# Kernel tuning notes

Hardware: AMD Instinct MI355X
Metric: run time of the kernel (lower is better)

## Reference

```python
import jax, jax.numpy as jnp
import numpy as np
from jax import lax

B, T, D, H = 4, 2048, 1024, 8
DK = D // H        # head qk dim (expand_k=1.0) = 128
DV = 2 * D // H    # head v dim (expand_v=2.0) = 256
C = 64             # retention chunk size


def setup_inputs() -> dict:
    key = jax.random.key(0)
    ks = jax.random.split(key, 7)
    s = 0.02
    return {
        "x": jax.random.normal(ks[0], (B, T, D), jnp.float32),
        "Wq": jax.random.normal(ks[1], (D, H * DK), jnp.float32) * s,
        "Wk": jax.random.normal(ks[2], (D, H * DK), jnp.float32) * s,
        "Wv": jax.random.normal(ks[3], (D, H * DV), jnp.float32) * s,
        "Wg": jax.random.normal(ks[4], (D, H * DV), jnp.float32) * s,
        "Wo": jax.random.normal(ks[5], (H * DV, D), jnp.float32) * s,
        "norm_w": jnp.ones((DV,), jnp.float32),
    }


def _rope(x):
    # x: [B,T,H,DK]; GPT-NeoX style (non-interleaved) rotary, base 10000
    half = DK // 2
    inv = 1.0 / (10000.0 ** (jnp.arange(0, DK, 2, dtype=jnp.float32) / DK))
    f = jnp.arange(T, dtype=jnp.float32)[:, None] * inv[None, :]  # [T, half]
    cos = jnp.cos(f)[None, :, None, :]
    sin = jnp.sin(f)[None, :, None, :]
    x1, x2 = x[..., :half], x[..., half:]
    return jnp.concatenate([x1 * cos - x2 * sin, x2 * cos + x1 * sin], axis=-1)


def _retention(q, k, v):
    # chunked decay-gated linear attention (RetNet retention)
    # q,k: [B,T,H,DK], v: [B,T,H,DV]; recurrence S_t = g*S_{t-1} + k_t^T v_t, o_t = q_t S_t
    N = T // C
    gamma = 1.0 - 2.0 ** (-5.0 - jnp.arange(H, dtype=jnp.float32))  # [H] per-head decay
    i = jnp.arange(C, dtype=jnp.float32)
    expo = i[:, None] - i[None, :]                                   # [C,C]
    M = jnp.where(expo >= 0, gamma[:, None, None] ** expo[None], 0.0)  # [H,C,C] intra-chunk decay mask
    dec_q = gamma[:, None] ** (i + 1.0)        # [H,C] decay of state seen by q_i
    dec_k = gamma[:, None] ** (C - 1.0 - i)    # [H,C] decay of k_j into end-of-chunk state
    gC = gamma ** C

    def to_chunks(t):
        return t.reshape(B, N, C, H, -1).transpose(1, 0, 3, 2, 4)  # [N,B,H,C,d]

    qs, kcs, vcs = to_chunks(q), to_chunks(k), to_chunks(v)

    def step(S, inp):
        qc, kc, vc = inp  # [B,H,C,DK],[B,H,C,DK],[B,H,C,DV]
        attn = jnp.einsum('bhid,bhjd->bhij', qc, kc) * M[None]
        o_intra = jnp.einsum('bhij,bhje->bhie', attn, vc)
        o_inter = jnp.einsum('bhid,bhde->bhie', qc, S) * dec_q[None, :, :, None]
        kv = jnp.einsum('bhjd,bhje->bhde', kc * dec_k[None, :, :, None], vc)
        S_new = gC[None, :, None, None] * S + kv
        return S_new, o_intra + o_inter

    S0 = jnp.zeros((B, H, DK, DV), q.dtype)
    _, os_ = lax.scan(step, S0, (qs, kcs, vcs))  # os_: [N,B,H,C,DV]
    return os_.transpose(1, 0, 3, 2, 4).reshape(B, T, H, DV)


def reference(x, Wq, Wk, Wv, Wg, Wo, norm_w):
    q = (x @ Wq).reshape(B, T, H, DK)
    k = (x @ Wk).reshape(B, T, H, DK)
    v = (x @ Wv).reshape(B, T, H, DV)
    g = (x @ Wg).reshape(B, T, H, DV)
    q, k = _rope(q), _rope(k)
    q = q * (DK ** -0.5)
    o = _retention(q, k, v)
    # fused per-head RMSNorm + swish output gate (FusedRMSNormSwishGate)
    rms = jnp.sqrt(jnp.mean(o * o, axis=-1, keepdims=True) + 1e-5)
    o = (o / rms) * norm_w
    o = o * g * jax.nn.sigmoid(g)
    return o.reshape(B, T, H * DV) @ Wo
```

## Files before the change

### kernel.cpp

```cpp
#include <hip/hip_runtime.h>
#include <hip/hip_bf16.h>
#include <cstdint>
#include <cstddef>

using f32x4 = __attribute__((ext_vector_type(4))) float;
using s16x8 = __attribute__((ext_vector_type(8))) short;
using s16x4 = __attribute__((ext_vector_type(4))) short;

#define DEVINL __device__ __forceinline__

static constexpr int T_LEN  = 2048;
static constexpr int MROWS  = 8192;
static constexpr int NCHUNK = 32;

DEVINL float bf2f(short s){
  unsigned u = ((unsigned)(unsigned short)s) << 16;
  return __builtin_bit_cast(float, u);
}
DEVINL short f2bf(float f){
  unsigned u = __builtin_bit_cast(unsigned, f);
  u = (u + 0x7fffu + ((u >> 16) & 1u)) >> 16;
  return (short)(unsigned short)u;
}

#define GLOAD16(gp, lp) \
  __builtin_amdgcn_global_load_lds((__attribute__((address_space(1))) void*)(gp), \
                                   (__attribute__((address_space(3))) void*)(lp), 16, 0, 0)

#define MFMA16(a, b, c) __builtin_amdgcn_mfma_f32_16x16x32_bf16((a), (b), (c), 0, 0, 0)
#define SBAR()  __builtin_amdgcn_sched_barrier(0)
#define WAITLGKM(n) asm volatile("s_waitcnt lgkmcnt(" #n ")" ::: "memory")
#define WAITVM(n)   asm volatile("s_waitcnt vmcnt(" #n ")" ::: "memory")

__global__ __launch_bounds__(256) void cvt_f32_bf16(const float* __restrict__ in,
                                                    short* __restrict__ out, int n4){
  int i = blockIdx.x * 256 + threadIdx.x;
  if (i >= n4) return;
  float4 v = ((const float4*)in)[i];
  short4 o;
  o.x = f2bf(v.x); o.y = f2bf(v.y); o.z = f2bf(v.z); o.w = f2bf(v.w);
  ((short4*)out)[i] = o;
}

__global__ __launch_bounds__(256) void tr_w(const float* __restrict__ in,
                                            short* __restrict__ out, int R, int C){
  __shared__ float tile[32][33];
  int c0 = blockIdx.x * 32, r0 = blockIdx.y * 32;
  int tx = threadIdx.x, ty = threadIdx.y;
  #pragma unroll
  for (int i = 0; i < 4; ++i){
    int r = ty + i * 8;
    tile[r][tx] = in[(size_t)(r0 + r) * C + c0 + tx];
  }
  __syncthreads();
  #pragma unroll
  for (int i = 0; i < 4; ++i){
    int c = ty + i * 8;
    out[(size_t)(c0 + c) * R + r0 + tx] = f2bf(tile[tx][c]);
  }
}

__global__ __launch_bounds__(256) void tr_k_decay(const short* __restrict__ in,
                                                  short* __restrict__ out){
  __shared__ float tile[32][33];
  int c0 = blockIdx.x * 32, r0 = blockIdx.y * 32;
  int tx = threadIdx.x, ty = threadIdx.y;
  #pragma unroll
  for (int i = 0; i < 4; ++i){
    int r = ty + i * 8;
    tile[r][tx] = bf2f(in[(size_t)(r0 + r) * 1024 + c0 + tx]);
  }
  __syncthreads();
  #pragma unroll
  for (int i = 0; i < 4; ++i){
    int c  = c0 + ty + i * 8;
    int h  = c >> 7;
    float lg = log2f(1.0f - exp2f(-(float)(5 + h)));
    int srow = r0 + tx;
    int j = srow & 63;
    float dec = exp2f((float)(63 - j) * lg);
    out[(size_t)c * MROWS + srow] = f2bf(tile[tx][ty + i * 8] * dec);
  }
}

__global__ __launch_bounds__(256) void rope_table(float* __restrict__ tab){
  int i = blockIdx.x * 256 + threadIdx.x;
  int t = i >> 6, d = i & 63;
  float inv = exp2f(-(float)d * (13.287712379549449f / 64.0f));
  float f = (float)t * inv;
  float s, c;
  sincosf(f, &s, &c);
  tab[2 * i]     = c;
  tab[2 * i + 1] = s;
}

__global__ __launch_bounds__(256) void rope_inplace(short* __restrict__ qk,
                                                    const float* __restrict__ tab,
                                                    float scale, int bake){
  int idx = blockIdx.x * 256 + threadIdx.x;
  int bt  = idx >> 9, rem = idx & 511;
  int h   = rem >> 6, d = rem & 63;
  int t   = bt & (T_LEN - 1);
  float2 cs = ((const float2*)tab)[t * 64 + d];
  float mult = scale;
  if (bake){
    float lg = log2f(1.0f - exp2f(-(float)(5 + h)));
    mult *= exp2f((float)((t & 63) + 1) * lg);
  }
  size_t base = (size_t)bt * 1024 + h * 128 + d;
  float x1 = bf2f(qk[base]), x2 = bf2f(qk[base + 64]);
  qk[base]      = f2bf((x1 * cs.x - x2 * cs.y) * mult);
  qk[base + 64] = f2bf((x2 * cs.x + x1 * cs.y) * mult);
}

DEVINL s16x8 frag64(const short* buf, int row, int ks, int lhi){
  int ch = (ks * 4 + lhi) ^ (row & 7);
  return *(const s16x8*)&buf[row * 64 + ch * 8];
}

template<int MODE>
__global__ __launch_bounds__(512, 2) void gemm256(const short* __restrict__ A,
                                                  const short* __restrict__ Bt,
                                                  void* __restrict__ o0, void* __restrict__ o1,
                                                  void* __restrict__ o2, void* __restrict__ o3,
                                                  int K, int nt, int NT){
  constexpr int BM   = (MODE == 2 ? 128 : 256);
  constexpr int ABUF = BM * 64;
  constexpr int MF   = BM / 32;
  constexpr int RPP  = MF / 4;
  __shared__ alignas(16) short LBUF[3 * ABUF + 2 * 16384];
  short* const BB = LBUF + 3 * ABUF;
  const int tid = threadIdx.x, wave = tid >> 6, lane = tid & 63;
  const int l15 = lane & 15, lhi = lane >> 4;
  const int wm = (wave >> 2) * (BM / 2), wn = (wave & 3) * 64;
  const int MG  = (gridDim.x >> 3) / NT;
  const int xcd = blockIdx.x & 7, idx = blockIdx.x >> 3;
  const int mi  = idx % MG, nn = idx / MG;
  const int m0  = (xcd * MG + mi) * BM, n0 = nn * 256;
  const short* Ag = A + (size_t)m0 * K;
  const short* Bg = Bt + (size_t)n0 * K;
  const int sr = lane >> 3;
  const int gc = ((lane & 7) ^ sr) * 8;
  const bool vreg = (MODE == 3) && (n0 >= 2048 && n0 < 4096);
  f32x4 acc[MF][4] = {};

  auto stageA = [&](int t, int half){
    short* lb = LBUF + (t % 3) * ABUF;
    size_t k0 = (size_t)t * 64;
    if constexpr (BM == 256){
      #pragma unroll
      for (int c = 0; c < 2; ++c){
        int r0 = half * 128 + c * 64;
        GLOAD16(Ag + (size_t)(r0 + wave * 8 + sr) * K + k0 + gc, lb + (r0 + wave * 8) * 64);
      }
    } else {
      int r0 = half * 64;
      GLOAD16(Ag + (size_t)(r0 + wave * 8 + sr) * K + k0 + gc, lb + (r0 + wave * 8) * 64);
    }
  };
  auto stageB = [&](int t, int half){
    short* lb = BB + (t & 1) * 16384;
    size_t k0 = (size_t)t * 64;
    #pragma unroll
    for (int c = 0; c < 2; ++c){
      int r0 = half * 128 + c * 64;
      GLOAD16(Bg + (size_t)(r0 + wave * 8 + sr) * K + k0 + gc, lb + (r0 + wave * 8) * 64);
    }
  };

  s16x8 bfr[2][4];
  s16x8 afA[RPP][2], afB[RPP][2];
  auto readAf = [&](s16x8 (&dst)[RPP][2], const short* Ab, int q){
    #pragma unroll
    for (int i = 0; i < RPP; ++i)
      #pragma unroll
      for (int ks = 0; ks < 2; ++ks)
        dst[i][ks] = frag64(Ab, wm + (RPP * q + i) * 16 + l15, ks, lhi);
  };
  auto readB = [&](const short* Bb){
    #pragma unroll
    for (int ks = 0; ks < 2; ++ks)
      #pragma unroll
      for (int nf = 0; nf < 4; ++nf)
        bfr[ks][nf] = frag64(Bb, wn + nf * 16 + l15, ks, lhi);
  };

  stageA(0, 0); stageA(0, 1); stageB(0, 0); stageB(0, 1);
  stageA(1, 0); stageA(1, 1); stageB(1, 0); stageB(1, 1);
  if constexpr (BM == 256) WAITVM(8); else WAITVM(6);
  SBAR();
  __builtin_amdgcn_s_barrier();
  readAf(afA, LBUF, 0);

  for (int t = 0; t < nt; ++t){
    const short* Ab  = LBUF + (t % 3) * ABUF;
    const short* Anx = LBUF + ((t + 1) % 3) * ABUF;
    const short* Bb  = BB + (t & 1) * 16384;
    #pragma unroll
    for (int q = 0; q < 4; ++q){
      __builtin_amdgcn_s_barrier();
      if (q == 2){
        if (t + 2 < nt){ if constexpr (BM == 256) WAITVM(4); else WAITVM(2); }
        else           { WAITVM(0); }
        SBAR();
      }
      if (t + 2 < nt){
        if (q == 0) stageA(t + 2, 0);
        if (q == 1) stageA(t + 2, 1);
        if (q == 2) stageB(t + 2, 0);
        if (q == 3) stageB(t + 2, 1);
      }
      bool tail = (q == 3) && (t + 1 >= nt);
      if (q == 0){ readB(Bb); SBAR(); readAf(afB, Ab, 1); }
      else if (q == 1){ readAf(afA, Ab, 2); }
      else if (q == 2){ readAf(afB, Ab, 3); }
      else if (!tail) { readAf(afA, Anx, 0); }
      if (tail){ WAITLGKM(0); }
      else if constexpr (RPP == 2){ WAITLGKM(4); }
      else                        { WAITLGKM(2); }
      SBAR();
      __builtin_amdgcn_s_setprio(1);
      if (vreg){
        #pragma unroll
        for (int i = 0; i < RPP; ++i)
          #pragma unroll
          for (int nf = 0; nf < 4; ++nf)
            #pragma unroll
            for (int ks = 0; ks < 2; ++ks)
              acc[RPP * q + i][nf] = (q & 1)
                ? MFMA16(afB[i][ks], bfr[ks][nf], acc[RPP * q + i][nf])
                : MFMA16(afA[i][ks], bfr[ks][nf], acc[RPP * q + i][nf]);
      } else {
        #pragma unroll
        for (int i = 0; i < RPP; ++i)
          #pragma unroll
          for (int nf = 0; nf < 4; ++nf)
            #pragma unroll
            for (int ks = 0; ks < 2; ++ks)
              acc[RPP * q + i][nf] = (q & 1)
                ? MFMA16(bfr[ks][nf], afB[i][ks], acc[RPP * q + i][nf])
                : MFMA16(bfr[ks][nf], afA[i][ks], acc[RPP * q + i][nf]);
      }
      __builtin_amdgcn_s_setprio(0);
    }
  }
  if (MODE == 2){
    float* dst = (float*)o0;
    #pragma unroll
    for (int mf = 0; mf < MF; ++mf){
      int m = m0 + wm + mf * 16 + l15;
      #pragma unroll
      for (int nf = 0; nf < 4; ++nf){
        int nb = n0 + wn + nf * 16 + 4 * lhi;
        *(float4*)&dst[(size_t)m * 1024 + nb] = *(float4*)&acc[mf][nf];
      }
    }
  } else if (vreg){
    short* dst = (short*)o2;
    #pragma unroll
    for (int mf = 0; mf < MF; ++mf){
      int rb = m0 + wm + mf * 16 + 4 * lhi;
      #pragma unroll
      for (int nf = 0; nf < 4; ++nf){
        int e = (n0 - 2048) + wn + nf * 16 + l15;
        s16x4 pk;
        #pragma unroll
        for (int r = 0; r < 4; ++r) pk[r] = f2bf(acc[mf][nf][r]);
        *(s16x4*)&dst[(size_t)e * MROWS + rb] = pk;
      }
    }
  } else {
    short* dst; int ld, cb;
    if (n0 < 1024)      { dst = (short*)o0; ld = 1024; cb = n0; }
    else if (n0 < 2048) { dst = (short*)o1; ld = 1024; cb = n0 - 1024; }
    else                { dst = (short*)o3; ld = 2048; cb = n0 - 4096; }
    #pragma unroll
    for (int mf = 0; mf < MF; ++mf){
      int m = m0 + wm + mf * 16 + l15;
      #pragma unroll
      for (int nf = 0; nf < 4; ++nf){
        int nb = cb + wn + nf * 16 + 4 * lhi;
        s16x4 pk;
        #pragma unroll
        for (int r = 0; r < 4; ++r) pk[r] = f2bf(acc[mf][nf][r]);
        *(s16x4*)&dst[(size_t)m * ld + nb] = pk;
      }
    }
  }
}

__global__ __launch_bounds__(256) void ret_scan(const short* __restrict__ kT,
                                                const short* __restrict__ vT,
                                                short* __restrict__ ST){
  __shared__ alignas(16) short kbuf[3][4096];
  __shared__ alignas(16) short vbuf[3][4096];
  const int tid = threadIdx.x, wave = tid >> 6, lane = tid & 63;
  const int db = blockIdx.x & 1, eb = blockIdx.x >> 1;
  const int h = blockIdx.y, b = blockIdx.z;
  const int d0 = db * 64, e0 = eb * 64;
  const float lg = log2f(1.0f - exp2f(-(float)(5 + h)));
  const float gC = exp2f(64.0f * lg);
  f32x4 Sacc[4] = {};
  const int srow = wave * 8 + (lane >> 3);
  const int sc   = lane & 7;

  auto STAGE = [&](int n, int buf){
    size_t rowbase = (size_t)(b * T_LEN + n * 64);
    #pragma unroll
    for (int c = 0; c < 2; ++c){
      int r = c * 32 + srow;
      int gc2 = sc ^ (r & 7);
      GLOAD16(kT + (size_t)(h * 128 + d0 + r) * MROWS + rowbase + gc2 * 8,
              &kbuf[buf][c * 2048 + wave * 512]);
    }
    #pragma unroll
    for (int c = 0; c < 2; ++c){
      int r = c * 32 + srow;
      int gc2 = sc ^ (r & 7);
      GLOAD16(vT + (size_t)(h * 256 + e0 + r) * MROWS + rowbase + gc2 * 8,
              &vbuf[buf][c * 2048 + wave * 512]);
    }
  };

  STAGE(0, 0);
  STAGE(1, 1);
  for (int n = 0; n < NCHUNK; ++n){
    const int buf = n % 3;
    if (n + 2 < NCHUNK) STAGE(n + 2, (n + 2) % 3);
    if (n > 0){
      size_t stb = (((size_t)n * 4 + b) * 8 + h) * 32768;
      int dbase = d0 + 16 * wave + 4 * (lane >> 4);
      #pragma unroll
      for (int nf = 0; nf < 4; ++nf){
        int e = e0 + nf * 16 + (lane & 15);
        s16x4 pk;
        #pragma unroll
        for (int r = 0; r < 4; ++r) pk[r] = f2bf(Sacc[nf][r]);
        *(s16x4*)&ST[stb + (size_t)e * 128 + dbase] = pk;
      }
    }
    if (n == 0)       WAITVM(8);
    else if (n < 30)  WAITVM(12);
    else if (n == 30) WAITVM(8);
    else              WAITVM(4);
    __builtin_amdgcn_s_barrier();
    SBAR();
    #pragma unroll
    for (int nf = 0; nf < 4; ++nf)
      #pragma unroll
      for (int r = 0; r < 4; ++r) Sacc[nf][r] *= gC;
    #pragma unroll
    for (int ks = 0; ks < 2; ++ks){
      int d = 16 * wave + (lane & 15);
      int chA = (ks * 4 + (lane >> 4)) ^ (d & 7);
      s16x8 af = *(const s16x8*)&kbuf[buf][d * 64 + chA * 8];
      #pragma unroll
      for (int nf = 0; nf < 4; ++nf){
        int e = nf * 16 + (lane & 15);
        int chB = (ks * 4 + (lane >> 4)) ^ (e & 7);
        s16x8 bv = *(const s16x8*)&vbuf[buf][e * 64 + chB * 8];
        Sacc[nf] = MFMA16(af, bv, Sacc[nf]);
      }
    }
    __builtin_amdgcn_s_barrier();
    SBAR();
  }
}

__global__ __launch_bounds__(256, 2) void ret_fused(const short* __restrict__ q,
                                                    const short* __restrict__ k,
                                                    const short* __restrict__ vT,
                                                    const short* __restrict__ ST,
                                                    const short* __restrict__ g,
                                                    const float* __restrict__ nw,
                                                    short* __restrict__ y){
  __shared__ alignas(16) short GS[16384];
  __shared__ alignas(16) float SS[256];
  __shared__ alignas(16) short XS[16896];
  short* PS = XS;
  short* YT = XS;
  const int tid = threadIdx.x, wave = tid >> 6, lane = tid & 63;
  const int l15 = lane & 15, lhi = lane >> 4;
  const int n = blockIdx.x, h = blockIdx.y, b = blockIdx.z;
  const size_t rowbase = (size_t)(b * T_LEN + n * 64);
  {
    int row = wave * 2 + (lane >> 5), sc32 = lane & 31;
    #pragma unroll
    for (int c = 0; c < 8; ++c){
      int r = c * 8 + row;
      GLOAD16(g + (rowbase + r) * 2048 + h * 256 + sc32 * 8, &GS[c * 2048 + wave * 512]);
    }
  }
  s16x8 Qf[4][4];
  #pragma unroll
  for (int rf = 0; rf < 4; ++rf)
    #pragma unroll
    for (int ks = 0; ks < 4; ++ks)
      Qf[rf][ks] = *(const s16x8*)&q[(rowbase + rf * 16 + l15) * 1024 + h * 128 + ks * 32 + lhi * 8];
  s16x8 Kf[4];
  #pragma unroll
  for (int ks = 0; ks < 4; ++ks)
    Kf[ks] = *(const s16x8*)&k[(rowbase + wave * 16 + l15) * 1024 + h * 128 + ks * 32 + lhi * 8];
  f32x4 accP[4] = {};
  #pragma unroll
  for (int ks = 0; ks < 4; ++ks)
    #pragma unroll
    for (int nf = 0; nf < 4; ++nf)
      accP[nf] = MFMA16(Kf[ks], Qf[nf][ks], accP[nf]);
  const float lg = log2f(1.0f - exp2f(-(float)(5 + h)));
  {
    int jb = wave * 16 + 4 * lhi;
    float dj[4];
    #pragma unroll
    for (int r = 0; r < 4; ++r) dj[r] = exp2f(-(float)(jb + r + 1) * lg);
    #pragma unroll
    for (int nf = 0; nf < 4; ++nf){
      int i = nf * 16 + l15;
      s16x4 pk;
      #pragma unroll
      for (int r = 0; r < 4; ++r)
        pk[r] = f2bf((i >= jb + r) ? accP[nf][r] * dj[r] : 0.0f);
      *(s16x4*)&PS[i * 72 + jb] = pk;
    }
  }
  f32x4 acc[4][4] = {};
  if (n){
    size_t stb = (((size_t)n * 4 + b) * 8 + h) * 32768;
    #pragma unroll
    for (int ks = 0; ks < 4; ++ks){
      s16x8 Sf[4];
      #pragma unroll
      for (int nf = 0; nf < 4; ++nf){
        int e = wave * 64 + nf * 16 + l15;
        Sf[nf] = *(const s16x8*)&ST[stb + (size_t)e * 128 + ks * 32 + lhi * 8];
      }
      #pragma unroll
      for (int mf = 0; mf < 4; ++mf)
        #pragma unroll
        for (int nf = 0; nf < 4; ++nf)
          acc[mf][nf] = MFMA16(Qf[mf][ks], Sf[nf], acc[mf][nf]);
    }
  }
  s16x8 Vf[2][4];
  #pragma unroll
  for (int ks2 = 0; ks2 < 2; ++ks2)
    #pragma unroll
    for (int nf = 0; nf < 4; ++nf){
      int e = wave * 64 + nf * 16 + l15;
      Vf[ks2][nf] = *(const s16x8*)&vT[(size_t)(h * 256 + e) * MROWS + rowbase + ks2 * 32 + lhi * 8];
    }
  __syncthreads();
  #pragma unroll
  for (int ks2 = 0; ks2 < 2; ++ks2){
    s16x8 Pf[4];
    #pragma unroll
    for (int mf = 0; mf < 4; ++mf)
      Pf[mf] = *(const s16x8*)&PS[(mf * 16 + l15) * 72 + ks2 * 32 + lhi * 8];
    #pragma unroll
    for (int mf = 0; mf < 4; ++mf)
      #pragma unroll
      for (int nf = 0; nf < 4; ++nf)
        acc[mf][nf] = MFMA16(Pf[mf], Vf[ks2][nf], acc[mf][nf]);
  }
  float ssp[4][4];
  #pragma unroll
  for (int mf = 0; mf < 4; ++mf)
    #pragma unroll
    for (int r = 0; r < 4; ++r){
      float s = 0.f;
      #pragma unroll
      for (int nf = 0; nf < 4; ++nf) s += acc[mf][nf][r] * acc[mf][nf][r];
      #pragma unroll
      for (int off = 8; off >= 1; off >>= 1) s += __shfl_xor(s, off, 64);
      ssp[mf][r] = s;
    }
  if (l15 == 0){
    #pragma unroll
    for (int mf = 0; mf < 4; ++mf)
      #pragma unroll
      for (int r = 0; r < 4; ++r){
        int row = mf * 16 + 4 * lhi + r;
        SS[row * 4 + wave] = ssp[mf][r];
      }
  }
  __syncthreads();
  #pragma unroll
  for (int mf = 0; mf < 4; ++mf){
    float rr[4];
    #pragma unroll
    for (int r = 0; r < 4; ++r){
      int row = mf * 16 + 4 * lhi + r;
      f32x4 s4 = *(const f32x4*)&SS[row * 4];
      float tot = s4[0] + s4[1] + s4[2] + s4[3];
      rr[r] = __builtin_amdgcn_rsqf(tot * (1.0f / 256.0f) + 1e-5f);
    }
    #pragma unroll
    for (int nf = 0; nf < 4; ++nf){
      int e = wave * 64 + nf * 16 + l15;
      float nwe = nw[e];
      #pragma unroll
      for (int r = 0; r < 4; ++r){
        int row = mf * 16 + 4 * lhi + r;
        float gf = bf2f(GS[row * 256 + e]);
        float sig = __builtin_amdgcn_rcpf(1.0f + exp2f(gf * -1.4426950408889634f));
        YT[row * 264 + e] = f2bf(acc[mf][nf][r] * rr[r] * nwe * gf * sig);
      }
    }
  }
  __syncthreads();
  #pragma unroll
  for (int it = 0; it < 8; ++it){
    int flat = it * 2048 + tid * 8;
    int row = flat >> 8, e = flat & 255;
    s16x8 v = *(const s16x8*)&YT[row * 264 + e];
    *(s16x8*)&y[(rowbase + row) * 2048 + h * 256 + e] = v;
  }
}

extern "C" void kernel_launch(void* const* d_in, const int* in_sizes, int n_in,
                              void* d_out, int out_size, void* d_ws, size_t ws_size,
                              hipStream_t stream){
  const float* x  = (const float*)d_in[0];
  const float* Wq = (const float*)d_in[1];
  const float* Wk = (const float*)d_in[2];
  const float* Wv = (const float*)d_in[3];
  const float* Wg = (const float*)d_in[4];
  const float* Wo = (const float*)d_in[5];
  const float* nw = (const float*)d_in[6];
  float* out = (float*)d_out;

  char* w = (char*)d_ws;
  short* xb  = (short*)w;               w += (size_t)8192 * 1024 * 2;
  short* WT  = (short*)w;               w += (size_t)6144 * 1024 * 2;
  short* kTt = (short*)w;               w += (size_t)1024 * 8192 * 2;
  short* qb  = (short*)w;               w += (size_t)8192 * 1024 * 2;
  short* kb  = (short*)w;               w += (size_t)8192 * 1024 * 2;
  short* vT  = (short*)w;               w += (size_t)2048 * 8192 * 2;
  short* gb  = (short*)w;               w += (size_t)8192 * 2048 * 2;
  short* STb = (short*)w;               w += (size_t)32 * 4 * 8 * 32768 * 2;
  short* WoT = (short*)w;               w += (size_t)1024 * 2048 * 2;
  short* yb  = (short*)d_ws;
  float* tab = (float*)STb;

  cvt_f32_bf16<<<8192, 256, 0, stream>>>(x, xb, 8192 * 1024 / 4);
  dim3 tb(32, 8);
  tr_w<<<dim3(32, 32), tb, 0, stream>>>(Wq, WT,                       1024, 1024);
  tr_w<<<dim3(32, 32), tb, 0, stream>>>(Wk, WT + (size_t)1024 * 1024, 1024, 1024);
  tr_w<<<dim3(64, 32), tb, 0, stream>>>(Wv, WT + (size_t)2048 * 1024, 1024, 2048);
  tr_w<<<dim3(64, 32), tb, 0, stream>>>(Wg, WT + (size_t)4096 * 1024, 1024, 2048);
  tr_w<<<dim3(32, 64), tb, 0, stream>>>(Wo, WoT,                      2048, 1024);
  rope_table<<<512, 256, 0, stream>>>(tab);

  gemm256<3><<<768, 512, 0, stream>>>(xb, WT, qb, kb, vT, gb, 1024, 16, 24);

  rope_inplace<<<16384, 256, 0, stream>>>(qb, tab, 0.08838834764831845f, 1);
  rope_inplace<<<16384, 256, 0, stream>>>(kb, tab, 1.0f, 0);
  tr_k_decay<<<dim3(32, 256), tb, 0, stream>>>(kb, kTt);

  ret_scan <<<dim3(8, 8, 4),  256, 0, stream>>>(kTt, vT, STb);
  ret_fused<<<dim3(32, 8, 4), 256, 0, stream>>>(qb, kb, vT, STb, gb, nw, yb);

  gemm256<2><<<256, 512, 0, stream>>>(yb, WoT, out, nullptr, nullptr, nullptr, 2048, 32, 4);
}
```

Before: 311.4 us.

## Split projection GEMM, merge weight transposes and rope launches, simplify GEMM pipeline

Merges the four QKVG weight transposes into one launch and the two RoPE launches into one 2D-grid launch. Reorders WT so Wg sits before Wv, and splits the fused QKVG GEMM into a q/k/g GEMM plus a separate MODE-4 GEMM that writes transposed v. This removes the runtime vreg branch. The GEMM main loop drops the register double-buffered A-fragment prefetch and uses simpler per-quarter fragment loads with a full LDS wait and barriers. That may lose overlap of LDS reads with MFMA work.

```diff
diff --git a/kernel.cpp b/kernel.cpp
--- a/kernel.cpp
+++ b/kernel.cpp
@@ -57,6 +57,33 @@
   for (int i = 0; i < 4; ++i){
     int c = ty + i * 8;
     out[(size_t)(c0 + c) * R + r0 + tx] = f2bf(tile[tx][c]);
+  }
+}
+
+__global__ __launch_bounds__(256) void tr_w4(const float* __restrict__ Wq,
+                                             const float* __restrict__ Wk,
+                                             const float* __restrict__ Wv,
+                                             const float* __restrict__ Wg,
+                                             short* __restrict__ WT){
+  __shared__ float tile[32][33];
+  int bx = blockIdx.x;
+  const float* src; int C; size_t off; int cb;
+  if (bx < 32)       { src = Wq; C = 1024; off = 0;                       cb = bx; }
+  else if (bx < 64)  { src = Wk; C = 1024; off = (size_t)1024 * 1024;     cb = bx - 32; }
+  else if (bx < 128) { src = Wg; C = 2048; off = (size_t)2048 * 1024;     cb = bx - 64; }
+  else               { src = Wv; C = 2048; off = (size_t)4096 * 1024;     cb = bx - 128; }
+  int c0 = cb * 32, r0 = blockIdx.y * 32;
+  int tx = threadIdx.x, ty = threadIdx.y;
+  #pragma unroll
+  for (int i = 0; i < 4; ++i){
+    int r = ty + i * 8;
+    tile[r][tx] = src[(size_t)(r0 + r) * C + c0 + tx];
+  }
+  __syncthreads();
+  #pragma unroll
+  for (int i = 0; i < 4; ++i){
+    int c = ty + i * 8;
+    WT[off + (size_t)(c0 + c) * 1024 + r0 + tx] = f2bf(tile[tx][c]);
   }
 }
 
@@ -94,23 +121,25 @@
   tab[2 * i + 1] = s;
 }
 
-__global__ __launch_bounds__(256) void rope_inplace(short* __restrict__ qk,
-                                                    const float* __restrict__ tab,
-                                                    float scale, int bake){
+__global__ __launch_bounds__(256) void rope2(short* __restrict__ qb, short* __restrict__ kb,
+                                             const float* __restrict__ tab){
   int idx = blockIdx.x * 256 + threadIdx.x;
   int bt  = idx >> 9, rem = idx & 511;
   int h   = rem >> 6, d = rem & 63;
   int t   = bt & (T_LEN - 1);
   float2 cs = ((const float2*)tab)[t * 64 + d];
-  float mult = scale;
-  if (bake){
+  short* dst; float mult;
+  if (blockIdx.y == 0){
+    dst = qb;
     float lg = log2f(1.0f - exp2f(-(float)(5 + h)));
-    mult *= exp2f((float)((t & 63) + 1) * lg);
+    mult = 0.08838834764831845f * exp2f((float)((t & 63) + 1) * lg);
+  } else {
+    dst = kb; mult = 1.0f;
   }
   size_t base = (size_t)bt * 1024 + h * 128 + d;
-  float x1 = bf2f(qk[base]), x2 = bf2f(qk[base + 64]);
-  qk[base]      = f2bf((x1 * cs.x - x2 * cs.y) * mult);
-  qk[base + 64] = f2bf((x2 * cs.x + x1 * cs.y) * mult);
+  float x1 = bf2f(dst[base]), x2 = bf2f(dst[base + 64]);
+  dst[base]      = f2bf((x1 * cs.x - x2 * cs.y) * mult);
+  dst[base + 64] = f2bf((x2 * cs.x + x1 * cs.y) * mult);
 }
 
 DEVINL s16x8 frag64(const short* buf, int row, int ks, int lhi){
@@ -141,7 +170,6 @@
   const short* Bg = Bt + (size_t)n0 * K;
   const int sr = lane >> 3;
   const int gc = ((lane & 7) ^ sr) * 8;
-  const bool vreg = (MODE == 3) && (n0 >= 2048 && n0 < 4096);
   f32x4 acc[MF][4] = {};
 
   auto stageA = [&](int t, int half){
@@ -166,23 +194,6 @@
       int r0 = half * 128 + c * 64;
       GLOAD16(Bg + (size_t)(r0 + wave * 8 + sr) * K + k0 + gc, lb + (r0 + wave * 8) * 64);
     }
-  };
-
-  s16x8 bfr[2][4];
-  s16x8 afA[RPP][2], afB[RPP][2];
-  auto readAf = [&](s16x8 (&dst)[RPP][2], const short* Ab, int q){
-    #pragma unroll
-    for (int i = 0; i < RPP; ++i)
-      #pragma unroll
-      for (int ks = 0; ks < 2; ++ks)
-        dst[i][ks] = frag64(Ab, wm + (RPP * q + i) * 16 + l15, ks, lhi);
-  };
-  auto readB = [&](const short* Bb){
-    #pragma unroll
-    for (int ks = 0; ks < 2; ++ks)
-      #pragma unroll
-      for (int nf = 0; nf < 4; ++nf)
-        bfr[ks][nf] = frag64(Bb, wn + nf * 16 + l15, ks, lhi);
   };
 
   stageA(0, 0); stageA(0, 1); stageB(0, 0); stageB(0, 1);
@@ -190,61 +201,61 @@
   if constexpr (BM == 256) WAITVM(8); else WAITVM(6);
   SBAR();
   __builtin_amdgcn_s_barrier();
-  readAf(afA, LBUF, 0);
 
   for (int t = 0; t < nt; ++t){
-    const short* Ab  = LBUF + (t % 3) * ABUF;
-    const short* Anx = LBUF + ((t + 1) % 3) * ABUF;
-    const short* Bb  = BB + (t & 1) * 16384;
+    const short* Ab = LBUF + (t % 3) * ABUF;
+    const short* Bb = BB + (t & 1) * 16384;
+    s16x8 bfr[2][4];
     #pragma unroll
     for (int q = 0; q < 4; ++q){
-      __builtin_amdgcn_s_barrier();
-      if (q == 2){
-        if (t + 2 < nt){ if constexpr (BM == 256) WAITVM(4); else WAITVM(2); }
-        else           { WAITVM(0); }
-        SBAR();
-      }
+      if (q == 0){
+        #pragma unroll
+        for (int ks = 0; ks < 2; ++ks)
+          #pragma unroll
+          for (int nf = 0; nf < 4; ++nf)
+            bfr[ks][nf] = frag64(Bb, wn + nf * 16 + l15, ks, lhi);
+      }
+      s16x8 af[RPP][2];
+      #pragma unroll
+      for (int i = 0; i < RPP; ++i)
+        #pragma unroll
+        for (int ks = 0; ks < 2; ++ks)
+          af[i][ks] = frag64(Ab, wm + (RPP * q + i) * 16 + l15, ks, lhi);
       if (t + 2 < nt){
         if (q == 0) stageA(t + 2, 0);
         if (q == 1) stageA(t + 2, 1);
         if (q == 2) stageB(t + 2, 0);
         if (q == 3) stageB(t + 2, 1);
       }
-      bool tail = (q == 3) && (t + 1 >= nt);
-      if (q == 0){ readB(Bb); SBAR(); readAf(afB, Ab, 1); }
-      else if (q == 1){ readAf(afA, Ab, 2); }
-      else if (q == 2){ readAf(afB, Ab, 3); }
-      else if (!tail) { readAf(afA, Anx, 0); }
-      if (tail){ WAITLGKM(0); }
-      else if constexpr (RPP == 2){ WAITLGKM(4); }
-      else                        { WAITLGKM(2); }
+      SBAR();
+      __builtin_amdgcn_s_barrier();
+      WAITLGKM(0);
       SBAR();
       __builtin_amdgcn_s_setprio(1);
-      if (vreg){
-        #pragma unroll
-        for (int i = 0; i < RPP; ++i)
+      #pragma unroll
+      for (int i = 0; i < RPP; ++i)
+        #pragma unroll
+        for (int nf = 0; nf < 4; ++nf)
           #pragma unroll
-          for (int nf = 0; nf < 4; ++nf)
-            #pragma unroll
-            for (int ks = 0; ks < 2; ++ks)
-              acc[RPP * q + i][nf] = (q & 1)
-                ? MFMA16(afB[i][ks], bfr[ks][nf], acc[RPP * q + i][nf])
-                : MFMA16(afA[i][ks], bfr[ks][nf], acc[RPP * q + i][nf]);
-      } else {
-        #pragma unroll
-        for (int i = 0; i < RPP; ++i)
-          #pragma unroll
-          for (int nf = 0; nf < 4; ++nf)
-            #pragma unroll
-            for (int ks = 0; ks < 2; ++ks)
-              acc[RPP * q + i][nf] = (q & 1)
-                ? MFMA16(bfr[ks][nf], afB[i][ks], acc[RPP * q + i][nf])
-                : MFMA16(bfr[ks][nf], afA[i][ks], acc[RPP * q + i][nf]);
-      }
+          for (int ks = 0; ks < 2; ++ks){
+            if constexpr (MODE == 4)
+              acc[RPP * q + i][nf] = MFMA16(af[i][ks], bfr[ks][nf], acc[RPP * q + i][nf]);
+            else
+              acc[RPP * q + i][nf] = MFMA16(bfr[ks][nf], af[i][ks], acc[RPP * q + i][nf]);
+          }
       __builtin_amdgcn_s_setprio(0);
-    }
-  }
-  if (MODE == 2){
+      if (q == 3){
+        if (t < nt - 2){
+          if constexpr (BM == 256) WAITVM(8); else WAITVM(6);
+        } else if (t == nt - 2){
+          WAITVM(0);
+        }
+        SBAR();
+      }
+      __builtin_amdgcn_s_barrier();
+    }
+  }
+  if constexpr (MODE == 2){
     float* dst = (float*)o0;
     #pragma unroll
     for (int mf = 0; mf < MF; ++mf){
@@ -255,14 +266,14 @@
         *(float4*)&dst[(size_t)m * 1024 + nb] = *(float4*)&acc[mf][nf];
       }
     }
-  } else if (vreg){
+  } else if constexpr (MODE == 4){
     short* dst = (short*)o2;
     #pragma unroll
     for (int mf = 0; mf < MF; ++mf){
       int rb = m0 + wm + mf * 16 + 4 * lhi;
       #pragma unroll
       for (int nf = 0; nf < 4; ++nf){
-        int e = (n0 - 2048) + wn + nf * 16 + l15;
+        int e = n0 + wn + nf * 16 + l15;
         s16x4 pk;
         #pragma unroll
         for (int r = 0; r < 4; ++r) pk[r] = f2bf(acc[mf][nf][r]);
@@ -273,7 +284,7 @@
     short* dst; int ld, cb;
     if (n0 < 1024)      { dst = (short*)o0; ld = 1024; cb = n0; }
     else if (n0 < 2048) { dst = (short*)o1; ld = 1024; cb = n0 - 1024; }
-    else                { dst = (short*)o3; ld = 2048; cb = n0 - 4096; }
+    else                { dst = (short*)o3; ld = 2048; cb = n0 - 2048; }
     #pragma unroll
     for (int mf = 0; mf < MF; ++mf){
       int m = m0 + wm + mf * 16 + l15;
@@ -544,17 +555,15 @@
 
   cvt_f32_bf16<<<8192, 256, 0, stream>>>(x, xb, 8192 * 1024 / 4);
   dim3 tb(32, 8);
-  tr_w<<<dim3(32, 32), tb, 0, stream>>>(Wq, WT,                       1024, 1024);
-  tr_w<<<dim3(32, 32), tb, 0, stream>>>(Wk, WT + (size_t)1024 * 1024, 1024, 1024);
-  tr_w<<<dim3(64, 32), tb, 0, stream>>>(Wv, WT + (size_t)2048 * 1024, 1024, 2048);
-  tr_w<<<dim3(64, 32), tb, 0, stream>>>(Wg, WT + (size_t)4096 * 1024, 1024, 2048);
-  tr_w<<<dim3(32, 64), tb, 0, stream>>>(Wo, WoT,                      2048, 1024);
+  tr_w4<<<dim3(192, 32), tb, 0, stream>>>(Wq, Wk, Wv, Wg, WT);
+  tr_w <<<dim3(32, 64),  tb, 0, stream>>>(Wo, WoT, 2048, 1024);
   rope_table<<<512, 256, 0, stream>>>(tab);
 
-  gemm256<3><<<768, 512, 0, stream>>>(xb, WT, qb, kb, vT, gb, 1024, 16, 24);
-
-  rope_inplace<<<16384, 256, 0, stream>>>(qb, tab, 0.08838834764831845f, 1);
-  rope_inplace<<<16384, 256, 0, stream>>>(kb, tab, 1.0f, 0);
+  gemm256<3><<<512, 512, 0, stream>>>(xb, WT, qb, kb, nullptr, gb, 1024, 16, 16);
+  gemm256<4><<<256, 512, 0, stream>>>(xb, WT + (size_t)4096 * 1024, nullptr, nullptr, vT, nullptr,
+                                      1024, 16, 8);
+
+  rope2<<<dim3(16384, 2), 256, 0, stream>>>(qb, kb, tab);
   tr_k_decay<<<dim3(32, 256), tb, 0, stream>>>(kb, kTt);
 
   ret_scan <<<dim3(8, 8, 4),  256, 0, stream>>>(kTt, vT, STb);
```

New measurement: 290.5 us. -6.7%, faster.
